# Optimization experiments

Hardware: AMD Instinct MI355X
Metric: run time of the kernel (lower is better)

## Reference

```python
import jax, jax.numpy as jnp
import numpy as np

BS, SEQ_LEN, N_NODES = 16, 12, 512
D, H, L, K = 256, 8, 2, 16
DFF = 4 * D
DH = D // H


def setup_inputs() -> dict:
    key = jax.random.key(0)
    ks = jax.random.split(key, 12)
    p = lambda i, shape: jax.random.normal(ks[i], shape, dtype=jnp.float32) * 0.02
    return dict(
        x_c=jax.random.normal(ks[0], (BS, SEQ_LEN, N_NODES), dtype=jnp.float32),
        A=jax.random.uniform(ks[1], (N_NODES, N_NODES), dtype=jnp.float32),
        W_src_emb=p(2, (SEQ_LEN, D)),
        W_tgt_emb=p(3, (SEQ_LEN, D)),
        enc_attn=p(4, (L, 4, D, D)),
        enc_ffn1=p(5, (L, D, DFF)),
        enc_ffn2=p(6, (L, DFF, D)),
        dec_self=p(7, (L, 4, D, D)),
        dec_cross=p(8, (L, 4, D, D)),
        dec_ffn1=p(9, (L, D, DFF)),
        dec_ffn2=p(10, (L, DFF, D)),
        W_gen=p(11, (D, SEQ_LEN)),
    )


def _ln(x):
    m = jnp.mean(x, axis=-1, keepdims=True)
    v = jnp.var(x, axis=-1, keepdims=True)
    return (x - m) * jax.lax.rsqrt(v + 1e-6)


def _mha(xq, xkv, W):
    # xq: [b, n, q, D], xkv: [b, n, s, D], W: [4, D, D]
    q = (xq @ W[0]).reshape(xq.shape[:-1] + (H, DH))
    k = (xkv @ W[1]).reshape(xkv.shape[:-1] + (H, DH))
    v = (xkv @ W[2]).reshape(xkv.shape[:-1] + (H, DH))
    sc = jnp.einsum('bnqhe,bnkhe->bnhqk', q, k) / np.float32(np.sqrt(DH))
    a = jax.nn.softmax(sc, axis=-1)
    o = jnp.einsum('bnhqk,bnkhe->bnqhe', a, v)
    o = o.reshape(o.shape[:-2] + (D,))
    return o @ W[3]


def _pe(length):
    pos = jnp.arange(length, dtype=jnp.float32)[:, None]
    div = jnp.exp(jnp.arange(0, D, 2, dtype=jnp.float32) * (-np.log(10000.0) / D))
    pe = jnp.zeros((length, D), dtype=jnp.float32)
    pe = pe.at[:, 0::2].set(jnp.sin(pos * div)).at[:, 1::2].set(jnp.cos(pos * div))
    return pe


def reference(x_c, A, W_src_emb, W_tgt_emb, enc_attn, enc_ffn1, enc_ffn2,
              dec_self, dec_cross, dec_ffn1, dec_ffn2, W_gen):
    # x_c: [bs, seq_len, N] -> x: [bs, N, seq_len]
    x = jnp.transpose(x_c, (0, 2, 1))
    # top-k neighbors per node (descending by A)
    index = jnp.argsort(-A, axis=-1)[:, :K]            # [N, K]
    sx = x[:, index]                                   # [bs, N, K, seq_len]  (the gather)
    tgt_in = x[:, :, None, :]                          # [bs, N, 1, seq_len]

    scale = np.float32(np.sqrt(D))
    src = sx @ W_src_emb * scale + _pe(K)              # [bs, N, K, D]
    tgt = tgt_in @ W_tgt_emb * scale + _pe(1)          # [bs, N, 1, D]

    # encoder (pre-norm residual sublayers, annotated-transformer style)
    for l in range(L):
        y = _ln(src)
        src = src + _mha(y, y, enc_attn[l])
        y = _ln(src)
        src = src + jax.nn.relu(y @ enc_ffn1[l]) @ enc_ffn2[l]
    memory = _ln(src)

    # decoder
    for l in range(L):
        y = _ln(tgt)
        tgt = tgt + _mha(y, y, dec_self[l])
        y = _ln(tgt)
        tgt = tgt + _mha(y, memory, dec_cross[l])
        y = _ln(tgt)
        tgt = tgt + jax.nn.relu(y @ dec_ffn1[l]) @ dec_ffn2[l]
    out = _ln(tgt) @ W_gen                             # [bs, N, 1, seq_len]
    return out[:, :, 0, :]                             # squeeze(-2): [bs, N, seq_len]
```

## Files before the change

### kernel.cpp

```cpp
#include <hip/hip_runtime.h>

typedef unsigned short u16;
typedef unsigned int u32;
typedef __attribute__((ext_vector_type(8))) short short8;
typedef __attribute__((ext_vector_type(4))) float f32x4;

__device__ __forceinline__ float bf2f(unsigned v){ union{unsigned u; float f;} c; c.u = v<<16; return c.f; }
__device__ __forceinline__ u16 f2bf(float f){
  union{float f; unsigned u;} c; c.f=f;
  unsigned u = c.u;
  u += 0x7fffu + ((u>>16)&1u);
  return (u16)(u>>16);
}
__device__ __forceinline__ float bfLO(u32 x){ union{u32 u; float f;} c; c.u = x<<16;        return c.f; }
__device__ __forceinline__ float bfHI(u32 x){ union{u32 u; float f;} c; c.u = x&0xffff0000u; return c.f; }

#define GLDS(g, l) __builtin_amdgcn_global_load_lds( \
    (const __attribute__((address_space(1))) void*)(g), \
    (__attribute__((address_space(3))) void*)(l), 16, 0, 0)

__global__ void topk_kernel(const float* __restrict__ A, int* __restrict__ idx){
  __shared__ float vals[512];
  const int n = blockIdx.x, t = threadIdx.x;
  for(int i=t;i<512;i+=64) vals[i] = A[n*512+i];
  __syncthreads();
  for(int kk=0;kk<16;kk++){
    float bv = -1e30f; int bi = 1<<30;
    for(int i=t;i<512;i+=64){
      float v = vals[i];
      if(v > bv){ bv=v; bi=i; }
    }
    #pragma unroll
    for(int off=32; off>0; off>>=1){
      float ov = __shfl_down(bv, off);
      int   oi = __shfl_down(bi, off);
      if(ov > bv || (ov==bv && oi<bi)){ bv=ov; bi=oi; }
    }
    bi = __shfl(bi, 0);
    if(t==0){ idx[n*16+kk] = bi; vals[bi] = -1e30f; }
    __syncthreads();
  }
}

__global__ __launch_bounds__(256)
void tcvt_kernel(const float* __restrict__ src, u16* __restrict__ dst, int R, int C){
  __shared__ float t[32][33];
  const int m = blockIdx.z;
  src += (size_t)m*R*C; dst += (size_t)m*R*C;
  const int c0 = blockIdx.x*32, r0 = blockIdx.y*32;
  const int tx = threadIdx.x, ty = threadIdx.y;
  #pragma unroll
  for(int i=0;i<4;i++) t[ty*4+i][tx] = src[(size_t)(r0+ty*4+i)*C + c0+tx];
  __syncthreads();
  #pragma unroll
  for(int i=0;i<4;i++) dst[(size_t)(c0+ty*4+i)*R + r0+tx] = f2bf(t[tx][ty*4+i]);
}

__global__ void cvt_kernel(const float* __restrict__ in, u16* __restrict__ out, int n4){
  int i = blockIdx.x*256 + threadIdx.x;
  if(i>=n4) return;
  float4 v = ((const float4*)in)[i];
  ushort4 o; o.x=f2bf(v.x); o.y=f2bf(v.y); o.z=f2bf(v.z); o.w=f2bf(v.w);
  ((ushort4*)out)[i] = o;
}

__global__ __launch_bounds__(256)
void embed_kernel(const float* __restrict__ x_c, const int* __restrict__ idx,
                  const float* __restrict__ Wsrc, const float* __restrict__ Wtgt,
                  u16* __restrict__ S, u16* __restrict__ SY,
                  u16* __restrict__ TGT, u16* __restrict__ TGTY, int g0){
  __shared__ float xs[16][12];
  __shared__ float xt[12];
  __shared__ float sm[16][260];
  __shared__ float mv[16][2];
  __shared__ float wpart[4][2];
  __shared__ float tmv[2];
  const int gl = blockIdx.x, g = gl + g0, b = g>>9, n = g&511, d = threadIdx.x;
  const int w = d>>6, lane = d&63;
  if(d < 192){ int kk=d/12, t=d-kk*12; xs[kk][t] = x_c[(b*12+t)*512 + idx[n*16+kk]]; }
  else if(d < 204){ int t=d-192; xt[t] = x_c[(b*12+t)*512 + n]; }
  __syncthreads();
  float wsr[12], wtg[12];
  #pragma unroll
  for(int t=0;t<12;t++){ wsr[t]=Wsrc[t*256+d]; wtg[t]=Wtgt[t*256+d]; }
  const float freq = expf(-(float)(d & ~1) * (9.210340371976184f/256.0f));
  const bool odd = d & 1;
  float xv[16];
  #pragma unroll
  for(int kk=0;kk<16;kk++){
    float a=0;
    #pragma unroll
    for(int t=0;t<12;t++) a = fmaf(xs[kk][t], wsr[t], a);
    float pe = odd ? cosf(freq*(float)kk) : sinf(freq*(float)kk);
    xv[kk] = a*16.0f + pe;
    S[(size_t)(gl*16+kk)*256 + d] = f2bf(xv[kk]);
    sm[kk][d] = xv[kk];
  }
  float tv;
  {
    float a=0;
    #pragma unroll
    for(int t=0;t<12;t++) a = fmaf(xt[t], wtg[t], a);
    tv = a*16.0f + (odd?1.0f:0.0f);
    TGT[(size_t)gl*256 + d] = f2bf(tv);
  }
  {
    float s2=tv, q2=tv*tv;
    #pragma unroll
    for(int off=32; off>0; off>>=1){ s2+=__shfl_xor(s2,off); q2+=__shfl_xor(q2,off); }
    if(lane==0){ wpart[w][0]=s2; wpart[w][1]=q2; }
  }
  __syncthreads();
  {
    const int kk=d>>4, part=d&15;
    float s=0,q=0;
    #pragma unroll
    for(int t=0;t<16;t++){ float v=sm[kk][part*16+t]; s+=v; q+=v*v; }
    #pragma unroll
    for(int off=1; off<16; off<<=1){ s+=__shfl_xor(s,off); q+=__shfl_xor(q,off); }
    if(part==0){
      float mean=s*(1.0f/256.0f);
      float var=q*(1.0f/256.0f)-mean*mean;
      mv[kk][0]=mean; mv[kk][1]=rsqrtf(var+1e-6f);
    }
    if(d==0){
      float ts=wpart[0][0]+wpart[1][0]+wpart[2][0]+wpart[3][0];
      float tq=wpart[0][1]+wpart[1][1]+wpart[2][1]+wpart[3][1];
      float mean=ts*(1.0f/256.0f);
      float var=tq*(1.0f/256.0f)-mean*mean;
      tmv[0]=mean; tmv[1]=rsqrtf(var+1e-6f);
    }
  }
  __syncthreads();
  #pragma unroll
  for(int kk=0;kk<16;kk++)
    SY[(size_t)(gl*16+kk)*256 + d] = f2bf((xv[kk]-mv[kk][0])*mv[kk][1]);
  TGTY[(size_t)gl*256 + d] = f2bf((tv-tmv[0])*tmv[1]);
}

template<int MODE>
__global__ __launch_bounds__(256)
void gemm_mfma(const u16* __restrict__ A, const u16* __restrict__ Bt, u16* __restrict__ C,
               int M, int N, int K)
{
  __shared__ u16 As[128*32];
  __shared__ u16 Bs[128*32];
  const int tid = threadIdx.x;
  const int w = tid>>6, l = tid&63;
  const int quad = l>>4, col16 = l&15;
  const int wr = (w>>1)*64, wc = (w&1)*64;
  const size_t m0 = (size_t)blockIdx.x*128;
  const size_t n0 = (size_t)blockIdx.y*128;

  const int sr = l>>2, sc = (l&3)*8;
  const int ca = w*2, cb = w*2+1;
  const u16* aG0 = A  + (m0 + ca*16 + sr)*K + sc;
  const u16* aG1 = A  + (m0 + cb*16 + sr)*K + sc;
  const u16* bG0 = Bt + (n0 + ca*16 + sr)*K + sc;
  const u16* bG1 = Bt + (n0 + cb*16 + sr)*K + sc;
  u16* aL0 = &As[ca*512];
  u16* aL1 = &As[cb*512];
  u16* bL0 = &Bs[ca*512];
  u16* bL1 = &Bs[cb*512];

  f32x4 acc[4][4];
  #pragma unroll
  for(int i=0;i<4;i++)
    #pragma unroll
    for(int j=0;j<4;j++) acc[i][j] = (f32x4){0.f,0.f,0.f,0.f};

  for(int k0=0;k0<K;k0+=32){
    GLDS(aG0 + k0, aL0);
    GLDS(aG1 + k0, aL1);
    GLDS(bG0 + k0, bL0);
    GLDS(bG1 + k0, bL1);
    __syncthreads();
    short8 af[4], bf[4];
    #pragma unroll
    for(int i=0;i<4;i++) af[i] = *(const short8*)&As[(wr + i*16 + col16)*32 + quad*8];
    #pragma unroll
    for(int j=0;j<4;j++) bf[j] = *(const short8*)&Bs[(wc + j*16 + col16)*32 + quad*8];
    #pragma unroll
    for(int i=0;i<4;i++)
      #pragma unroll
      for(int j=0;j<4;j++)
        acc[i][j] = __builtin_amdgcn_mfma_f32_16x16x32_bf16(af[i], bf[j], acc[i][j], 0,0,0);
    __syncthreads();
  }

  #pragma unroll
  for(int i=0;i<4;i++){
    #pragma unroll
    for(int r=0;r<4;r++){
      const size_t row = m0 + wr + i*16 + quad*4 + r;
      u16* cp = C + row*(size_t)N + n0 + wc + col16;
      #pragma unroll
      for(int j=0;j<4;j++){
        float v = acc[i][j][r];
        if(MODE==2) v += bf2f(cp[j*16]);
        if(MODE==1) v = fmaxf(v, 0.f);
        cp[j*16] = f2bf(v);
      }
    }
  }
}

template<int MODE>
__global__ __launch_bounds__(256,2)
void gemm_wide(const u16* __restrict__ A, const u16* __restrict__ Bt, u16* __restrict__ C,
               int M, int N, int K)
{
  __shared__ u16 As[128*32];
  __shared__ u16 Bs[256*32];
  const int tid = threadIdx.x;
  const int w = tid>>6, l = tid&63;
  const int quad = l>>4, col16 = l&15;
  const int wr = (w>>1)*64, wc = (w&1)*128;
  const size_t m0 = (size_t)blockIdx.x*128;
  const size_t n0 = (size_t)blockIdx.y*256;

  const int sr = l>>2, sc = (l&3)*8;
  const u16* aG0 = A + (m0 + (w*2+0)*16 + sr)*K + sc;
  const u16* aG1 = A + (m0 + (w*2+1)*16 + sr)*K + sc;
  u16* aL0 = &As[(w*2+0)*512];
  u16* aL1 = &As[(w*2+1)*512];
  const u16* bG[4]; u16* bL[4];
  #pragma unroll
  for(int c=0;c<4;c++){
    int ch = w*4+c;
    bG[c] = Bt + (n0 + ch*16 + sr)*K + sc;
    bL[c] = &Bs[ch*512];
  }

  f32x4 acc[4][8];
  #pragma unroll
  for(int i=0;i<4;i++)
    #pragma unroll
    for(int j=0;j<8;j++) acc[i][j] = (f32x4){0.f,0.f,0.f,0.f};

  for(int k0=0;k0<K;k0+=32){
    GLDS(aG0 + k0, aL0);
    GLDS(aG1 + k0, aL1);
    #pragma unroll
    for(int c=0;c<4;c++) GLDS(bG[c] + k0, bL[c]);
    __syncthreads();
    short8 af[4], bf[8];
    #pragma unroll
    for(int i=0;i<4;i++) af[i] = *(const short8*)&As[(wr + i*16 + col16)*32 + quad*8];
    #pragma unroll
    for(int j=0;j<8;j++) bf[j] = *(const short8*)&Bs[(wc + j*16 + col16)*32 + quad*8];
    #pragma unroll
    for(int i=0;i<4;i++)
      #pragma unroll
      for(int j=0;j<8;j++)
        acc[i][j] = __builtin_amdgcn_mfma_f32_16x16x32_bf16(af[i], bf[j], acc[i][j], 0,0,0);
    __syncthreads();
  }

  #pragma unroll
  for(int i=0;i<4;i++){
    #pragma unroll
    for(int r=0;r<4;r++){
      const size_t row = m0 + wr + i*16 + quad*4 + r;
      u16* cp = C + row*(size_t)N + n0 + wc + col16;
      #pragma unroll
      for(int j=0;j<8;j++){
        float v = acc[i][j][r];
        if(MODE==1) v = fmaxf(v, 0.f);
        cp[j*16] = f2bf(v);
      }
    }
  }
}

__global__ __launch_bounds__(256,2)
void gemm_addln(const u16* __restrict__ A, const u16* __restrict__ Bt,
                u16* __restrict__ C, u16* __restrict__ Y, int M, int K)
{
  __shared__ u16 As[128*32];
  __shared__ u16 Bs[256*32];
  __shared__ float ssum[128][2];
  __shared__ float ssq[128][2];
  const int tid = threadIdx.x;
  const int w = tid>>6, l = tid&63;
  const int quad = l>>4, col16 = l&15;
  const int wr = (w>>1)*64, wc = (w&1)*128;
  const int wh = w&1;
  const size_t m0 = (size_t)blockIdx.x*128;

  const int sr = l>>2, sc = (l&3)*8;
  const u16* aG0 = A + (m0 + (w*2+0)*16 + sr)*K + sc;
  const u16* aG1 = A + (m0 + (w*2+1)*16 + sr)*K + sc;
  u16* aL0 = &As[(w*2+0)*512];
  u16* aL1 = &As[(w*2+1)*512];
  const u16* bG[4]; u16* bL[4];
  #pragma unroll
  for(int c=0;c<4;c++){
    int ch = w*4+c;
    bG[c] = Bt + (size_t)(ch*16 + sr)*K + sc;
    bL[c] = &Bs[ch*512];
  }

  f32x4 acc[4][8];
  #pragma unroll
  for(int i=0;i<4;i++)
    #pragma unroll
    for(int j=0;j<8;j++) acc[i][j] = (f32x4){0.f,0.f,0.f,0.f};

  for(int k0=0;k0<K;k0+=32){
    GLDS(aG0 + k0, aL0);
    GLDS(aG1 + k0, aL1);
    #pragma unroll
    for(int c=0;c<4;c++) GLDS(bG[c] + k0, bL[c]);
    __syncthreads();
    short8 af[4], bf[8];
    #pragma unroll
    for(int i=0;i<4;i++) af[i] = *(const short8*)&As[(wr + i*16 + col16)*32 + quad*8];
    #pragma unroll
    for(int j=0;j<8;j++) bf[j] = *(const short8*)&Bs[(wc + j*16 + col16)*32 + quad*8];
    #pragma unroll
    for(int i=0;i<4;i++)
      #pragma unroll
      for(int j=0;j<8;j++)
        acc[i][j] = __builtin_amdgcn_mfma_f32_16x16x32_bf16(af[i], bf[j], acc[i][j], 0,0,0);
    __syncthreads();
  }

  #pragma unroll
  for(int i=0;i<4;i++){
    #pragma unroll
    for(int r=0;r<4;r++){
      const int lr = wr + i*16 + quad*4 + r;
      const u16* cp = C + (m0 + lr)*(size_t)256 + wc + col16;
      float s=0.f, q=0.f;
      #pragma unroll
      for(int j=0;j<8;j++){
        float v = acc[i][j][r] + bf2f(cp[j*16]);
        acc[i][j][r] = v;
        s += v; q += v*v;
      }
      #pragma unroll
      for(int off=1; off<16; off<<=1){ s+=__shfl_xor(s,off); q+=__shfl_xor(q,off); }
      if(col16==0){ ssum[lr][wh]=s; ssq[lr][wh]=q; }
    }
  }
  __syncthreads();
  #pragma unroll
  for(int i=0;i<4;i++){
    #pragma unroll
    for(int r=0;r<4;r++){
      const int lr = wr + i*16 + quad*4 + r;
      const float mean = (ssum[lr][0]+ssum[lr][1])*(1.0f/256.0f);
      const float var  = (ssq[lr][0]+ssq[lr][1])*(1.0f/256.0f) - mean*mean;
      const float rs   = rsqrtf(var + 1e-6f);
      u16* cp = C + (m0 + lr)*(size_t)256 + wc + col16;
      u16* yp = Y + (m0 + lr)*(size_t)256 + wc + col16;
      #pragma unroll
      for(int j=0;j<8;j++){
        float v = acc[i][j][r];
        cp[j*16] = f2bf(v);
        yp[j*16] = f2bf((v-mean)*rs);
      }
    }
  }
}

__global__ __launch_bounds__(256)
void attn_enc_kernel(const u16* __restrict__ QKV, u16* __restrict__ O){
  __shared__ u16 sb[12672];
  const int tid = threadIdx.x;
  const size_t g = blockIdx.x;
  const size_t grow = g*16;
  #pragma unroll
  for(int it=0; it<6; it++){
    int e = (tid + 256*it)*8;
    int r = e/768, c = e - r*768;
    int t = c>>8, cc = c&255;
    *(uint4*)&sb[t*4224 + r*264 + cc] = *(const uint4*)&QKV[(grow+r)*768 + c];
  }
  __syncthreads();
  const int h = tid>>5, q = (tid>>1)&15, eh = tid&1;
  const int eo = h*32 + eh*16;
  float qv[16];
  #pragma unroll
  for(int e2=0;e2<8;e2++){
    u32 x = *(const u32*)&sb[q*264 + eo + e2*2];
    qv[2*e2]=bfLO(x); qv[2*e2+1]=bfHI(x);
  }
  float sc[16];
  #pragma unroll
  for(int kk=0;kk<16;kk++){
    const u16* kr = &sb[4224 + kk*264 + eo];
    float s=0;
    #pragma unroll
    for(int e2=0;e2<8;e2++){
      u32 x = *(const u32*)&kr[e2*2];
      s = fmaf(qv[2*e2], bfLO(x), s);
      s = fmaf(qv[2*e2+1], bfHI(x), s);
    }
    s += __shfl_xor(s, 1);
    sc[kk] = s*0.17677669529663687f;
  }
  float m=sc[0];
  #pragma unroll
  for(int kk=1;kk<16;kk++) m=fmaxf(m,sc[kk]);
  float sum=0;
  #pragma unroll
  for(int kk=0;kk<16;kk++){ sc[kk]=expf(sc[kk]-m); sum+=sc[kk]; }
  float inv=1.0f/sum;
  float ov[16];
  #pragma unroll
  for(int e=0;e<16;e++) ov[e]=0.f;
  #pragma unroll
  for(int kk=0;kk<16;kk++){
    float p = sc[kk]*inv;
    const u16* vr = &sb[8448 + kk*264 + eo];
    #pragma unroll
    for(int e2=0;e2<8;e2++){
      u32 x = *(const u32*)&vr[e2*2];
      ov[2*e2]   = fmaf(p, bfLO(x), ov[2*e2]);
      ov[2*e2+1] = fmaf(p, bfHI(x), ov[2*e2+1]);
    }
  }
  u16* op = O + (grow+q)*256 + eo;
  #pragma unroll
  for(int b=0;b<4;b++){
    ushort4 t4; t4.x=f2bf(ov[4*b]); t4.y=f2bf(ov[4*b+1]); t4.z=f2bf(ov[4*b+2]); t4.w=f2bf(ov[4*b+3]);
    *(ushort4*)&op[b*4] = t4;
  }
}

__global__ __launch_bounds__(256)
void attn_cross_kernel(const u16* __restrict__ Qc, const u16* __restrict__ KV,
                       u16* __restrict__ Oc, int loff){
  __shared__ float qs[256];
  __shared__ float ks[16*264], vs[16*264];
  __shared__ float aw[128];
  const int t = threadIdx.x;
  const size_t g = blockIdx.x;
  qs[t] = bf2f(Qc[g*256+t]);
  for(int i=t;i<4096;i+=256){
    int r=i>>8, c=i&255;
    int li = r*264 + ((c>>5)*33) + (c&31);
    const u16* p = KV + (g*16+r)*1024 + loff + c;
    ks[li]=bf2f(p[0]); vs[li]=bf2f(p[256]);
  }
  __syncthreads();
  if(t<128){
    int h=t>>4, kk=t&15;
    float s=0;
    #pragma unroll
    for(int e=0;e<32;e++) s = fmaf(qs[h*32+e], ks[kk*264+h*33+e], s);
    aw[h*16+kk] = s*0.17677669529663687f;
  }
  __syncthreads();
  if(t<8){
    float m=-1e30f;
    for(int kk=0;kk<16;kk++) m=fmaxf(m, aw[t*16+kk]);
    float sum=0;
    for(int kk=0;kk<16;kk++){ float e=expf(aw[t*16+kk]-m); aw[t*16+kk]=e; sum+=e; }
    float inv=1.0f/sum;
    for(int kk=0;kk<16;kk++) aw[t*16+kk]*=inv;
  }
  __syncthreads();
  {
    int h=t>>5, e=t&31;
    float o=0;
    #pragma unroll
    for(int kk=0;kk<16;kk++) o = fmaf(aw[h*16+kk], vs[kk*264+h*33+e], o);
    Oc[g*256+t] = f2bf(o);
  }
}

__global__ __launch_bounds__(64)
void final_kernel(const u16* __restrict__ TY, const float* __restrict__ Wg, float* __restrict__ out, int g0){
  __shared__ float y[256];
  const int lane = threadIdx.x;
  const size_t gl = blockIdx.x;
  ushort4 u = *(const ushort4*)(TY + gl*256 + (size_t)lane*4);
  y[lane*4+0]=bf2f(u.x); y[lane*4+1]=bf2f(u.y); y[lane*4+2]=bf2f(u.z); y[lane*4+3]=bf2f(u.w);
  __syncthreads();
  if(lane<12){
    float s=0;
    for(int d=0;d<256;d++) s = fmaf(y[d], Wg[d*12+lane], s);
    out[(g0+gl)*12+lane]=s;
  }
}

extern "C" void kernel_launch(void* const* d_in, const int* in_sizes, int n_in,
                              void* d_out, int out_size, void* d_ws, size_t ws_size,
                              hipStream_t stream)
{
  (void)in_sizes; (void)n_in; (void)out_size;
  const float* x_c  = (const float*)d_in[0];
  const float* A    = (const float*)d_in[1];
  const float* Wsrc = (const float*)d_in[2];
  const float* Wtgt = (const float*)d_in[3];
  const float* wsrc_f[7] = {(const float*)d_in[4],(const float*)d_in[5],(const float*)d_in[6],
                            (const float*)d_in[7],(const float*)d_in[8],(const float*)d_in[9],
                            (const float*)d_in[10]};
  const float* W_gen = (const float*)d_in[11];
  float* out = (float*)d_out;

  auto align256 = [](size_t b)->size_t{ return (b + 255) & ~(size_t)255; };
  auto need_bytes = [&](int GC)->size_t{
    size_t b = 0;
    b += align256(512*16*4);
    for(int i=0;i<7;i++) b += align256((size_t)524288*2);
    b += align256((size_t)4*65536*2);
    b += align256((size_t)2*65536*2)*2;
    b += align256((size_t)GC*16*256*2)*2;
    b += align256((size_t)GC*16*1024*2);
    b += align256((size_t)GC*256*2)*4;
    b += align256((size_t)GC*1024*2);
    return b;
  };
  int GC = 8192;
  while(GC > 128 && need_bytes(GC) > ws_size) GC >>= 1;

  char* ws = (char*)d_ws;
  size_t off = 0;
  auto alloc = [&](size_t bytes)->char*{
    char* p = ws + off;
    off += (bytes + 255) & ~(size_t)255;
    return p;
  };
  int* idx = (int*)alloc(512*16*4);
  u16* wt[7];
  for(int i=0;i<7;i++) wt[i] = (u16*)alloc((size_t)524288*2);
  u16* wKV      = (u16*)alloc((size_t)4*65536*2);
  u16* wv_plain = (u16*)alloc((size_t)2*65536*2);
  u16* wVO      = (u16*)alloc((size_t)2*65536*2);
  u16* cS  = (u16*)alloc((size_t)GC*16*256*2);
  u16* cY  = (u16*)alloc((size_t)GC*16*256*2);
  u16* big = (u16*)alloc((size_t)GC*16*1024*2);
  u16* tgt = (u16*)alloc((size_t)GC*256*2);
  u16* tY  = (u16*)alloc((size_t)GC*256*2);
  u16* tA  = (u16*)alloc((size_t)GC*256*2);
  u16* tO  = (u16*)alloc((size_t)GC*256*2);
  u16* tT  = (u16*)alloc((size_t)GC*1024*2);

  u16* wQKV = big;
  u16* Tc   = big;
  u16* KVc  = big;

  {
    dim3 blk(32,8);
    tcvt_kernel<<<dim3( 256/32, 256/32, 8), blk, 0, stream>>>(wsrc_f[0], wt[0], 256, 256);
    tcvt_kernel<<<dim3(1024/32, 256/32, 2), blk, 0, stream>>>(wsrc_f[1], wt[1], 256,1024);
    tcvt_kernel<<<dim3( 256/32,1024/32, 2), blk, 0, stream>>>(wsrc_f[2], wt[2],1024, 256);
    tcvt_kernel<<<dim3( 256/32, 256/32, 8), blk, 0, stream>>>(wsrc_f[3], wt[3], 256, 256);
    tcvt_kernel<<<dim3( 256/32, 256/32, 8), blk, 0, stream>>>(wsrc_f[4], wt[4], 256, 256);
    tcvt_kernel<<<dim3(1024/32, 256/32, 2), blk, 0, stream>>>(wsrc_f[5], wt[5], 256,1024);
    tcvt_kernel<<<dim3( 256/32,1024/32, 2), blk, 0, stream>>>(wsrc_f[6], wt[6],1024, 256);
  }
  topk_kernel<<<512,64,0,stream>>>(A, idx);

  hipMemcpyAsync(wKV+0*65536, wt[4]+1*65536, 65536*2, hipMemcpyDeviceToDevice, stream);
  hipMemcpyAsync(wKV+1*65536, wt[4]+2*65536, 65536*2, hipMemcpyDeviceToDevice, stream);
  hipMemcpyAsync(wKV+2*65536, wt[4]+5*65536, 65536*2, hipMemcpyDeviceToDevice, stream);
  hipMemcpyAsync(wKV+3*65536, wt[4]+6*65536, 65536*2, hipMemcpyDeviceToDevice, stream);

  for(int l=0;l<2;l++){
    cvt_kernel<<<64,256,0,stream>>>(wsrc_f[3]+(size_t)(l*4+2)*65536, wv_plain+(size_t)l*65536, 16384);
    gemm_mfma<0><<<dim3(2,2),256,0,stream>>>(wt[3]+(size_t)(l*4+3)*65536, wv_plain+(size_t)l*65536,
                                             wVO+(size_t)l*65536, 256,256,256);
  }

  auto gemm = [&](const u16* Am, const u16* Bm, u16* Cm, int M_, int N_, int K_, int mode){
    dim3 grid(M_/128, N_/128);
    if(mode==1)      gemm_mfma<1><<<grid,256,0,stream>>>(Am,Bm,Cm,M_,N_,K_);
    else if(mode==2) gemm_mfma<2><<<grid,256,0,stream>>>(Am,Bm,Cm,M_,N_,K_);
    else             gemm_mfma<0><<<grid,256,0,stream>>>(Am,Bm,Cm,M_,N_,K_);
  };
  auto gemmw = [&](const u16* Am, const u16* Bm, u16* Cm, int M_, int N_, int K_, int mode){
    dim3 grid(M_/128, N_/256);
    if(mode==1) gemm_wide<1><<<grid,256,0,stream>>>(Am,Bm,Cm,M_,N_,K_);
    else        gemm_wide<0><<<grid,256,0,stream>>>(Am,Bm,Cm,M_,N_,K_);
  };
  auto gemm_ln = [&](const u16* Am, const u16* Bm, u16* Cm, u16* Ym, int M_, int K_){
    gemm_addln<<<dim3(M_/128),256,0,stream>>>(Am,Bm,Cm,Ym,M_,K_);
  };

  const int Mr = GC*16;
  const int Md = GC;

  for(int g0=0; g0<8192; g0+=GC){
    embed_kernel<<<GC,256,0,stream>>>(x_c, idx, Wsrc, Wtgt, cS, cY, tgt, tY, g0);

    for(int l=0;l<2;l++){
      const u16* Wat = wt[0] + (size_t)l*4*65536;
      gemmw(cY, Wat, wQKV, Mr, 768, 256, 0);
      attn_enc_kernel<<<GC,256,0,stream>>>(wQKV, cY);
      gemm_ln(cY, Wat+3*65536, cS, cY, Mr, 256);
      gemmw(cY, wt[1]+(size_t)l*262144, Tc, Mr,1024, 256, 1);
      gemm_ln(Tc, wt[2]+(size_t)l*262144, cS, cY, Mr, 1024);
    }
    gemmw(cY, wKV, KVc, Mr, 1024, 256, 0);

    for(int l=0;l<2;l++){
      const u16* Wdc = wt[4] + (size_t)l*4*65536;
      gemm_ln(tY, wVO+(size_t)l*65536, tgt, tY, Md, 256);
      gemm(tY, Wdc, tA, Md, 256, 256, 0);
      attn_cross_kernel<<<GC,256,0,stream>>>(tA, KVc, tO, l*512);
      gemm_ln(tO, Wdc+3*65536, tgt, tY, Md, 256);
      gemmw(tY, wt[5]+(size_t)l*262144, tT, Md,1024, 256, 1);
      gemm_ln(tT, wt[6]+(size_t)l*262144, tgt, tY, Md, 1024);
    }

    final_kernel<<<GC,64,0,stream>>>(tY, W_gen, out, g0);
  }
}
```

Before: 1.720 ms.

## Fuse FFN up-projection, ReLU, down-projection and add+LayerNorm into one kernel

Adds a fused FFN kernel that computes each 64-row tile's 1024-wide hidden activation in 64-column chunks held in shared memory and feeds it straight into the down-projection, then does the residual add and LayerNorm. This removes the round trip of the large hidden tensor through global memory and one kernel launch per FFN. It also swaps grid axes in the GEMMs so consecutive blocks share the same A rows. The cost is that weights are re-streamed from global/L2 by every block, the loop has many barriers with no double buffering, and each block gets less MFMA work per load.

```diff
diff --git a/kernel.cpp b/kernel.cpp
--- a/kernel.cpp
+++ b/kernel.cpp
@@ -149,8 +149,8 @@
   const int w = tid>>6, l = tid&63;
   const int quad = l>>4, col16 = l&15;
   const int wr = (w>>1)*64, wc = (w&1)*64;
-  const size_t m0 = (size_t)blockIdx.x*128;
-  const size_t n0 = (size_t)blockIdx.y*128;
+  const size_t m0 = (size_t)blockIdx.y*128;
+  const size_t n0 = (size_t)blockIdx.x*128;
 
   const int sr = l>>2, sc = (l&3)*8;
   const int ca = w*2, cb = w*2+1;
@@ -216,8 +216,8 @@
   const int w = tid>>6, l = tid&63;
   const int quad = l>>4, col16 = l&15;
   const int wr = (w>>1)*64, wc = (w&1)*128;
-  const size_t m0 = (size_t)blockIdx.x*128;
-  const size_t n0 = (size_t)blockIdx.y*256;
+  const size_t m0 = (size_t)blockIdx.y*128;
+  const size_t n0 = (size_t)blockIdx.x*256;
 
   const int sr = l>>2, sc = (l&3)*8;
   const u16* aG0 = A + (m0 + (w*2+0)*16 + sr)*K + sc;
@@ -366,6 +366,120 @@
 }
 
 __global__ __launch_bounds__(256)
+void ffn_fused(const u16* __restrict__ Y, const u16* __restrict__ F1t, const u16* __restrict__ F2t,
+               u16* __restrict__ C, u16* __restrict__ Yout, int M)
+{
+  __shared__ u16 ys[32*64*8];
+  __shared__ u16 wbuf[16384];
+  __shared__ u16 ss[8*64*8];
+  __shared__ float ssum[64][4], ssq[64][4];
+  const int tid = threadIdx.x;
+  const int w = tid>>6, l = tid&63;
+  const int quad = l>>4, col16 = l&15;
+  const size_t m0 = (size_t)blockIdx.x*64;
+
+  #pragma unroll
+  for(int t=0;t<8;t++){
+    int kb = t*4 + w;
+    GLDS(Y + (m0 + l)*256 + kb*8, &ys[kb*512]);
+  }
+
+  f32x4 acc[4][4];
+  #pragma unroll
+  for(int i=0;i<4;i++)
+    #pragma unroll
+    for(int j=0;j<4;j++) acc[i][j] = (f32x4){0.f,0.f,0.f,0.f};
+
+  for(int c=0;c<16;c++){
+    __syncthreads();
+    #pragma unroll
+    for(int t=0;t<8;t++){
+      int kb = t*4 + w;
+      GLDS(F1t + (size_t)(c*64 + l)*256 + kb*8, &wbuf[kb*512]);
+    }
+    __syncthreads();
+    f32x4 accs[4];
+    #pragma unroll
+    for(int j=0;j<4;j++) accs[j] = (f32x4){0.f,0.f,0.f,0.f};
+    #pragma unroll
+    for(int kt=0;kt<8;kt++){
+      short8 a = *(const short8*)&ys[((kt*4+quad)*64 + w*16 + col16)*8];
+      #pragma unroll
+      for(int j=0;j<4;j++){
+        short8 b = *(const short8*)&wbuf[((kt*4+quad)*64 + j*16 + col16)*8];
+        accs[j] = __builtin_amdgcn_mfma_f32_16x16x32_bf16(a, b, accs[j], 0,0,0);
+      }
+    }
+    #pragma unroll
+    for(int j=0;j<4;j++){
+      #pragma unroll
+      for(int r=0;r<4;r++){
+        int m = w*16 + quad*4 + r;
+        int k = j*16 + col16;
+        ss[((k>>3)*64 + m)*8 + (k&7)] = f2bf(fmaxf(accs[j][r], 0.f));
+      }
+    }
+    __syncthreads();
+    #pragma unroll
+    for(int kb=0;kb<8;kb++){
+      GLDS(F2t + (size_t)(w*64 + l)*1024 + c*64 + kb*8, &wbuf[(kb*256 + w*64)*8]);
+    }
+    __syncthreads();
+    #pragma unroll
+    for(int kt=0;kt<2;kt++){
+      short8 a[4], b[4];
+      #pragma unroll
+      for(int i=0;i<4;i++) a[i] = *(const short8*)&ss[((kt*4+quad)*64 + i*16 + col16)*8];
+      #pragma unroll
+      for(int j=0;j<4;j++) b[j] = *(const short8*)&wbuf[((kt*4+quad)*256 + w*64 + j*16 + col16)*8];
+      #pragma unroll
+      for(int i=0;i<4;i++)
+        #pragma unroll
+        for(int j=0;j<4;j++)
+          acc[i][j] = __builtin_amdgcn_mfma_f32_16x16x32_bf16(a[i], b[j], acc[i][j], 0,0,0);
+    }
+  }
+
+  #pragma unroll
+  for(int i=0;i<4;i++){
+    #pragma unroll
+    for(int r=0;r<4;r++){
+      const int m = i*16 + quad*4 + r;
+      const u16* cp = C + (m0 + m)*(size_t)256 + w*64 + col16;
+      float s=0.f, q=0.f;
+      #pragma unroll
+      for(int j=0;j<4;j++){
+        float v = acc[i][j][r] + bf2f(cp[j*16]);
+        acc[i][j][r] = v;
+        s += v; q += v*v;
+      }
+      #pragma unroll
+      for(int off=1; off<16; off<<=1){ s+=__shfl_xor(s,off); q+=__shfl_xor(q,off); }
+      if(col16==0){ ssum[m][w]=s; ssq[m][w]=q; }
+    }
+  }
+  __syncthreads();
+  #pragma unroll
+  for(int i=0;i<4;i++){
+    #pragma unroll
+    for(int r=0;r<4;r++){
+      const int m = i*16 + quad*4 + r;
+      const float mean = (ssum[m][0]+ssum[m][1]+ssum[m][2]+ssum[m][3])*(1.0f/256.0f);
+      const float var  = (ssq[m][0]+ssq[m][1]+ssq[m][2]+ssq[m][3])*(1.0f/256.0f) - mean*mean;
+      const float rs   = rsqrtf(var + 1e-6f);
+      u16* cp = C    + (m0 + m)*(size_t)256 + w*64 + col16;
+      u16* yp = Yout + (m0 + m)*(size_t)256 + w*64 + col16;
+      #pragma unroll
+      for(int j=0;j<4;j++){
+        float v = acc[i][j][r];
+        cp[j*16] = f2bf(v);
+        yp[j*16] = f2bf((v-mean)*rs);
+      }
+    }
+  }
+}
+
+__global__ __launch_bounds__(256)
 void attn_enc_kernel(const u16* __restrict__ QKV, u16* __restrict__ O){
   __shared__ u16 sb[12672];
   const int tid = threadIdx.x;
@@ -512,7 +626,6 @@
     b += align256((size_t)GC*16*256*2)*2;
     b += align256((size_t)GC*16*1024*2);
     b += align256((size_t)GC*256*2)*4;
-    b += align256((size_t)GC*1024*2);
     return b;
   };
   int GC = 8192;
@@ -538,10 +651,8 @@
   u16* tY  = (u16*)alloc((size_t)GC*256*2);
   u16* tA  = (u16*)alloc((size_t)GC*256*2);
   u16* tO  = (u16*)alloc((size_t)GC*256*2);
-  u16* tT  = (u16*)alloc((size_t)GC*1024*2);
 
   u16* wQKV = big;
-  u16* Tc   = big;
   u16* KVc  = big;
 
   {
@@ -568,19 +679,22 @@
   }
 
   auto gemm = [&](const u16* Am, const u16* Bm, u16* Cm, int M_, int N_, int K_, int mode){
-    dim3 grid(M_/128, N_/128);
+    dim3 grid(N_/128, M_/128);
     if(mode==1)      gemm_mfma<1><<<grid,256,0,stream>>>(Am,Bm,Cm,M_,N_,K_);
     else if(mode==2) gemm_mfma<2><<<grid,256,0,stream>>>(Am,Bm,Cm,M_,N_,K_);
     else             gemm_mfma<0><<<grid,256,0,stream>>>(Am,Bm,Cm,M_,N_,K_);
   };
   auto gemmw = [&](const u16* Am, const u16* Bm, u16* Cm, int M_, int N_, int K_, int mode){
-    dim3 grid(M_/128, N_/256);
+    dim3 grid(N_/256, M_/128);
     if(mode==1) gemm_wide<1><<<grid,256,0,stream>>>(Am,Bm,Cm,M_,N_,K_);
     else        gemm_wide<0><<<grid,256,0,stream>>>(Am,Bm,Cm,M_,N_,K_);
   };
   auto gemm_ln = [&](const u16* Am, const u16* Bm, u16* Cm, u16* Ym, int M_, int K_){
     gemm_addln<<<dim3(M_/128),256,0,stream>>>(Am,Bm,Cm,Ym,M_,K_);
   };
+  auto ffn = [&](const u16* Ym, const u16* F1, const u16* F2, u16* Cm, u16* Yo, int M_){
+    ffn_fused<<<dim3(M_/64),256,0,stream>>>(Ym,F1,F2,Cm,Yo,M_);
+  };
 
   const int Mr = GC*16;
   const int Md = GC;
@@ -593,8 +707,7 @@
       gemmw(cY, Wat, wQKV, Mr, 768, 256, 0);
       attn_enc_kernel<<<GC,256,0,stream>>>(wQKV, cY);
       gemm_ln(cY, Wat+3*65536, cS, cY, Mr, 256);
-      gemmw(cY, wt[1]+(size_t)l*262144, Tc, Mr,1024, 256, 1);
-      gemm_ln(Tc, wt[2]+(size_t)l*262144, cS, cY, Mr, 1024);
+      ffn(cY, wt[1]+(size_t)l*262144, wt[2]+(size_t)l*262144, cS, cY, Mr);
     }
     gemmw(cY, wKV, KVc, Mr, 1024, 256, 0);
 
@@ -604,8 +717,7 @@
       gemm(tY, Wdc, tA, Md, 256, 256, 0);
       attn_cross_kernel<<<GC,256,0,stream>>>(tA, KVc, tO, l*512);
       gemm_ln(tO, Wdc+3*65536, tgt, tY, Md, 256);
-      gemmw(tY, wt[5]+(size_t)l*262144, tT, Md,1024, 256, 1);
-      gemm_ln(tT, wt[6]+(size_t)l*262144, tgt, tY, Md, 1024);
+      ffn(tY, wt[5]+(size_t)l*262144, wt[6]+(size_t)l*262144, tgt, tY, Md);
     }
 
     final_kernel<<<GC,64,0,stream>>>(tY, W_gen, out, g0);
```

Result: slower. 2.020 ms (+17.5%).

## Fold cross-attention K/V projections into per-head query and output weights

Applied to the files above, without the earlier changes.

Cross-attention no longer projects the encoder memory to K and V. Wq·Wk^T is folded per head into a 256x2048 matrix so scores are computed directly against the raw memory. Wv·Wo is folded into a 2048x256 matrix applied after attention-weighted memory sums. This removes the large Mr x 1024 KV GEMM per chunk. In exchange the decoder-side GEMMs grow (N=2048 and K=2048 on only GC rows) and the attention kernel reads the full 256-dim memory per head. GEMM grid axes are also swapped so that N tiles vary fastest.

```diff
diff --git a/kernel.cpp b/kernel.cpp
--- a/kernel.cpp
+++ b/kernel.cpp
@@ -62,6 +62,39 @@
   float4 v = ((const float4*)in)[i];
   ushort4 o; o.x=f2bf(v.x); o.y=f2bf(v.y); o.z=f2bf(v.z); o.w=f2bf(v.w);
   ((ushort4*)out)[i] = o;
+}
+
+__global__ __launch_bounds__(256)
+void foldq_kernel(const float* __restrict__ Wq, const float* __restrict__ Wk,
+                  u16* __restrict__ out){
+  __shared__ float kv[32];
+  const int n = blockIdx.x, h = n>>8, d = n&255, f = threadIdx.x;
+  if(f<32) kv[f] = Wk[d*256 + h*32 + f];
+  __syncthreads();
+  const float* wq = Wq + f*256 + h*32;
+  float s=0;
+  #pragma unroll
+  for(int e=0;e<32;e++) s = fmaf(kv[e], wq[e], s);
+  out[(size_t)n*256 + f] = f2bf(s);
+}
+
+__global__ __launch_bounds__(256)
+void foldv_kernel(const float* __restrict__ Wv, const float* __restrict__ Wo,
+                  u16* __restrict__ out){
+  __shared__ float ws[256];
+  const int dp = blockIdx.x;
+  const int t = threadIdx.x;
+  ws[t] = Wo[t*256 + dp];
+  __syncthreads();
+  for(int n=t;n<2048;n+=256){
+    int h=n>>8, d=n&255;
+    const float* wv = Wv + d*256 + h*32;
+    const float* wo = &ws[h*32];
+    float s=0;
+    #pragma unroll
+    for(int e=0;e<32;e++) s = fmaf(wv[e], wo[e], s);
+    out[(size_t)dp*2048 + n] = f2bf(s);
+  }
 }
 
 __global__ __launch_bounds__(256)
@@ -149,8 +182,8 @@
   const int w = tid>>6, l = tid&63;
   const int quad = l>>4, col16 = l&15;
   const int wr = (w>>1)*64, wc = (w&1)*64;
-  const size_t m0 = (size_t)blockIdx.x*128;
-  const size_t n0 = (size_t)blockIdx.y*128;
+  const size_t m0 = (size_t)blockIdx.y*128;
+  const size_t n0 = (size_t)blockIdx.x*128;
 
   const int sr = l>>2, sc = (l&3)*8;
   const int ca = w*2, cb = w*2+1;
@@ -216,8 +249,8 @@
   const int w = tid>>6, l = tid&63;
   const int quad = l>>4, col16 = l&15;
   const int wr = (w>>1)*64, wc = (w&1)*128;
-  const size_t m0 = (size_t)blockIdx.x*128;
-  const size_t n0 = (size_t)blockIdx.y*256;
+  const size_t m0 = (size_t)blockIdx.y*128;
+  const size_t n0 = (size_t)blockIdx.x*256;
 
   const int sr = l>>2, sc = (l&3)*8;
   const u16* aG0 = A + (m0 + (w*2+0)*16 + sr)*K + sc;
@@ -431,44 +464,64 @@
 }
 
 __global__ __launch_bounds__(256)
-void attn_cross_kernel(const u16* __restrict__ Qc, const u16* __restrict__ KV,
-                       u16* __restrict__ Oc, int loff){
-  __shared__ float qs[256];
-  __shared__ float ks[16*264], vs[16*264];
+void attn_cross2(const u16* __restrict__ Qt, const u16* __restrict__ MEM,
+                 u16* __restrict__ Mb){
+  __shared__ float qs[8][260];
+  __shared__ float ms[16*264];
   __shared__ float aw[128];
   const int t = threadIdx.x;
   const size_t g = blockIdx.x;
-  qs[t] = bf2f(Qc[g*256+t]);
+  const u32* qp = (const u32*)(Qt + g*2048);
+  for(int i=t;i<1024;i+=256){
+    u32 x = qp[i];
+    int h = i>>7, dd = (i&127)*2;
+    qs[h][dd] = bfLO(x); qs[h][dd+1] = bfHI(x);
+  }
   for(int i=t;i<4096;i+=256){
     int r=i>>8, c=i&255;
-    int li = r*264 + ((c>>5)*33) + (c&31);
-    const u16* p = KV + (g*16+r)*1024 + loff + c;
-    ks[li]=bf2f(p[0]); vs[li]=bf2f(p[256]);
+    ms[r*264 + (c>>5)*33 + (c&31)] = bf2f(MEM[(g*16+r)*256 + c]);
   }
   __syncthreads();
   if(t<128){
-    int h=t>>4, kk=t&15;
+    int h=t>>4, j=t&15;
     float s=0;
     #pragma unroll
-    for(int e=0;e<32;e++) s = fmaf(qs[h*32+e], ks[kk*264+h*33+e], s);
-    aw[h*16+kk] = s*0.17677669529663687f;
+    for(int d5=0;d5<8;d5++){
+      const float* mp = &ms[j*264 + d5*33];
+      const float* qq = &qs[h][d5*32];
+      #pragma unroll
+      for(int e=0;e<32;e++) s = fmaf(qq[e], mp[e], s);
+    }
+    aw[h*16+j] = s*0.17677669529663687f;
   }
   __syncthreads();
   if(t<8){
     float m=-1e30f;
-    for(int kk=0;kk<16;kk++) m=fmaxf(m, aw[t*16+kk]);
+    for(int j=0;j<16;j++) m=fmaxf(m, aw[t*16+j]);
     float sum=0;
-    for(int kk=0;kk<16;kk++){ float e=expf(aw[t*16+kk]-m); aw[t*16+kk]=e; sum+=e; }
+    for(int j=0;j<16;j++){ float e=expf(aw[t*16+j]-m); aw[t*16+j]=e; sum+=e; }
     float inv=1.0f/sum;
-    for(int kk=0;kk<16;kk++) aw[t*16+kk]*=inv;
+    for(int j=0;j<16;j++) aw[t*16+j]*=inv;
   }
   __syncthreads();
   {
-    int h=t>>5, e=t&31;
-    float o=0;
-    #pragma unroll
-    for(int kk=0;kk<16;kk++) o = fmaf(aw[h*16+kk], vs[kk*264+h*33+e], o);
-    Oc[g*256+t] = f2bf(o);
+    const int h=t>>5, d0=(t&31)*8;
+    const int lo = (d0>>5)*33 + (d0&31);
+    float acc[8];
+    #pragma unroll
+    for(int i=0;i<8;i++) acc[i]=0.f;
+    #pragma unroll
+    for(int j=0;j<16;j++){
+      float p = aw[h*16+j];
+      const float* mp = &ms[j*264 + lo];
+      #pragma unroll
+      for(int i=0;i<8;i++) acc[i] = fmaf(p, mp[i], acc[i]);
+    }
+    u16* op = Mb + g*2048 + h*256 + d0;
+    ushort4 a,b;
+    a.x=f2bf(acc[0]); a.y=f2bf(acc[1]); a.z=f2bf(acc[2]); a.w=f2bf(acc[3]);
+    b.x=f2bf(acc[4]); b.y=f2bf(acc[5]); b.z=f2bf(acc[6]); b.w=f2bf(acc[7]);
+    *(ushort4*)op = a; *(ushort4*)&op[4] = b;
   }
 }
 
@@ -507,7 +560,8 @@
     size_t b = 0;
     b += align256(512*16*4);
     for(int i=0;i<7;i++) b += align256((size_t)524288*2);
-    b += align256((size_t)4*65536*2);
+    b += align256((size_t)524288*2)*2;
+    b += align256((size_t)524288*2)*2;
     b += align256((size_t)2*65536*2)*2;
     b += align256((size_t)GC*16*256*2)*2;
     b += align256((size_t)GC*16*1024*2);
@@ -528,7 +582,8 @@
   int* idx = (int*)alloc(512*16*4);
   u16* wt[7];
   for(int i=0;i<7;i++) wt[i] = (u16*)alloc((size_t)524288*2);
-  u16* wKV      = (u16*)alloc((size_t)4*65536*2);
+  u16* wQt  = (u16*)alloc((size_t)524288*2*2);
+  u16* wVOc = (u16*)alloc((size_t)524288*2*2);
   u16* wv_plain = (u16*)alloc((size_t)2*65536*2);
   u16* wVO      = (u16*)alloc((size_t)2*65536*2);
   u16* cS  = (u16*)alloc((size_t)GC*16*256*2);
@@ -539,10 +594,12 @@
   u16* tA  = (u16*)alloc((size_t)GC*256*2);
   u16* tO  = (u16*)alloc((size_t)GC*256*2);
   u16* tT  = (u16*)alloc((size_t)GC*1024*2);
+  (void)tA; (void)tO;
 
   u16* wQKV = big;
   u16* Tc   = big;
-  u16* KVc  = big;
+  u16* tQ   = big;
+  u16* tM   = big + (size_t)GC*2048;
 
   {
     dim3 blk(32,8);
@@ -550,16 +607,16 @@
     tcvt_kernel<<<dim3(1024/32, 256/32, 2), blk, 0, stream>>>(wsrc_f[1], wt[1], 256,1024);
     tcvt_kernel<<<dim3( 256/32,1024/32, 2), blk, 0, stream>>>(wsrc_f[2], wt[2],1024, 256);
     tcvt_kernel<<<dim3( 256/32, 256/32, 8), blk, 0, stream>>>(wsrc_f[3], wt[3], 256, 256);
-    tcvt_kernel<<<dim3( 256/32, 256/32, 8), blk, 0, stream>>>(wsrc_f[4], wt[4], 256, 256);
     tcvt_kernel<<<dim3(1024/32, 256/32, 2), blk, 0, stream>>>(wsrc_f[5], wt[5], 256,1024);
     tcvt_kernel<<<dim3( 256/32,1024/32, 2), blk, 0, stream>>>(wsrc_f[6], wt[6],1024, 256);
   }
   topk_kernel<<<512,64,0,stream>>>(A, idx);
 
-  hipMemcpyAsync(wKV+0*65536, wt[4]+1*65536, 65536*2, hipMemcpyDeviceToDevice, stream);
-  hipMemcpyAsync(wKV+1*65536, wt[4]+2*65536, 65536*2, hipMemcpyDeviceToDevice, stream);
-  hipMemcpyAsync(wKV+2*65536, wt[4]+5*65536, 65536*2, hipMemcpyDeviceToDevice, stream);
-  hipMemcpyAsync(wKV+3*65536, wt[4]+6*65536, 65536*2, hipMemcpyDeviceToDevice, stream);
+  for(int l=0;l<2;l++){
+    const float* Wb = wsrc_f[4] + (size_t)l*4*65536;
+    foldq_kernel<<<2048,256,0,stream>>>(Wb+0*65536, Wb+1*65536, wQt + (size_t)l*524288);
+    foldv_kernel<<< 256,256,0,stream>>>(Wb+2*65536, Wb+3*65536, wVOc + (size_t)l*524288);
+  }
 
   for(int l=0;l<2;l++){
     cvt_kernel<<<64,256,0,stream>>>(wsrc_f[3]+(size_t)(l*4+2)*65536, wv_plain+(size_t)l*65536, 16384);
@@ -567,14 +624,8 @@
                                              wVO+(size_t)l*65536, 256,256,256);
   }
 
-  auto gemm = [&](const u16* Am, const u16* Bm, u16* Cm, int M_, int N_, int K_, int mode){
-    dim3 grid(M_/128, N_/128);
-    if(mode==1)      gemm_mfma<1><<<grid,256,0,stream>>>(Am,Bm,Cm,M_,N_,K_);
-    else if(mode==2) gemm_mfma<2><<<grid,256,0,stream>>>(Am,Bm,Cm,M_,N_,K_);
-    else             gemm_mfma<0><<<grid,256,0,stream>>>(Am,Bm,Cm,M_,N_,K_);
-  };
   auto gemmw = [&](const u16* Am, const u16* Bm, u16* Cm, int M_, int N_, int K_, int mode){
-    dim3 grid(M_/128, N_/256);
+    dim3 grid(N_/256, M_/128);
     if(mode==1) gemm_wide<1><<<grid,256,0,stream>>>(Am,Bm,Cm,M_,N_,K_);
     else        gemm_wide<0><<<grid,256,0,stream>>>(Am,Bm,Cm,M_,N_,K_);
   };
@@ -596,14 +647,12 @@
       gemmw(cY, wt[1]+(size_t)l*262144, Tc, Mr,1024, 256, 1);
       gemm_ln(Tc, wt[2]+(size_t)l*262144, cS, cY, Mr, 1024);
     }
-    gemmw(cY, wKV, KVc, Mr, 1024, 256, 0);
 
     for(int l=0;l<2;l++){
-      const u16* Wdc = wt[4] + (size_t)l*4*65536;
       gemm_ln(tY, wVO+(size_t)l*65536, tgt, tY, Md, 256);
-      gemm(tY, Wdc, tA, Md, 256, 256, 0);
-      attn_cross_kernel<<<GC,256,0,stream>>>(tA, KVc, tO, l*512);
-      gemm_ln(tO, Wdc+3*65536, tgt, tY, Md, 256);
+      gemmw(tY, wQt + (size_t)l*524288, tQ, Md, 2048, 256, 0);
+      attn_cross2<<<GC,256,0,stream>>>(tQ, cY, tM);
+      gemm_ln(tM, wVOc + (size_t)l*524288, tgt, tY, Md, 2048);
       gemmw(tY, wt[5]+(size_t)l*262144, tT, Md,1024, 256, 1);
       gemm_ln(tT, wt[6]+(size_t)l*262144, tgt, tY, Md, 1024);
     }
```

Result: slower. 1.954 ms (+13.6%).
